# Kernel tuning notes

Hardware: AMD Instinct MI355X
Metric: run time of the kernel (lower is better)

## Reference

```python
import jax, jax.numpy as jnp
import numpy as np

N = 100000       # num nodes
E = 1600000      # num edges
D_IN = 32
D_HID = 32
D_OUT = 32
K = 3            # Chebyshev order (number of terms)


def setup_inputs() -> dict:
    key = jax.random.key(0)
    k1, k2, k3, k4, k5, k6 = jax.random.split(key, 6)
    x = jax.random.normal(k1, (N, D_IN), dtype=jnp.float32)
    edge_index = jax.random.randint(k2, (2, E), 0, N, dtype=jnp.int64)
    s1 = 1.0 / np.sqrt(D_IN)
    s2 = 1.0 / np.sqrt(D_HID)
    W1 = jax.random.uniform(k3, (K, D_IN, D_HID), jnp.float32, -s1, s1)
    b1 = jax.random.uniform(k4, (D_HID,), jnp.float32, -s1, s1)
    W2 = jax.random.uniform(k5, (K, D_HID, D_OUT), jnp.float32, -s2, s2)
    b2 = jax.random.uniform(k6, (D_OUT,), jnp.float32, -s2, s2)
    return {"x": x, "edge_index": edge_index, "W1": W1, "b1": b1, "W2": W2, "b2": b2}


def _prop(x, row, col, w):
    # L_hat @ x : gather along col, scale by edge weight, scatter-add to row.
    # (diagonal of the rescaled Laplacian cancels to 0 in PyG ChebConv with
    #  sym normalization and lambda_max=2, so only off-diagonal edges remain)
    return jax.ops.segment_sum(w[:, None] * x[col], row, num_segments=N)


def _cheb_conv(x, row, col, w, W, b):
    # Chebyshev recurrence: Tx0 = x, Tx1 = L_hat x, Tx_k = 2 L_hat Tx_{k-1} - Tx_{k-2}
    k_terms = W.shape[0]
    Tx0 = x
    out = Tx0 @ W[0]
    if k_terms > 1:
        Tx1 = _prop(Tx0, row, col, w)
        out = out + Tx1 @ W[1]
        for k in range(2, k_terms):
            Tx2 = 2.0 * _prop(Tx1, row, col, w) - Tx0
            out = out + Tx2 @ W[k]
            Tx0, Tx1 = Tx1, Tx2
    return out + b


def reference(x, edge_index, W1, b1, W2, b2):
    row, col = edge_index[0], edge_index[1]
    mask = (row != col).astype(x.dtype)            # remove_self_loops
    deg = jax.ops.segment_sum(mask, row, num_segments=N)
    dinv = jnp.where(deg > 0, 1.0 / jnp.sqrt(jnp.maximum(deg, 1.0)), 0.0)
    w = -mask * dinv[row] * dinv[col]              # scaled Laplacian off-diagonal weights
    x0 = x
    h = jax.nn.relu(_cheb_conv(x, row, col, w, W1, b1))
    h = _cheb_conv(h, row, col, w, W2, b2)
    return h + x0
```

## Files before the change

kernel.cpp:

```cpp
#include <hip/hip_runtime.h>

#define NN 100000
#define EE 1600000
#define DD 32
#define NBUK 391
#define BROWS 256
#define TILE 4096
#define NT 391
#define BCAP2 4864

#define TOTP   106176
#define ENT2SZ 2084352
#define ZTOT   ((TOTP * 16 + ENT2SZ * 4) / 16)
#define ZPB    ((ZTOT + NT - 1) / NT)

__constant__ int c_cap[9]   = {0, 2944, 56320, 43520, 2944, 256, 64, 64, 64};
__constant__ int c_pbase[9] = {0, 0, 2944, 59264, 102784, 105728, 105984, 106048, 106112};
__constant__ int c_ebase[9] = {0, 0, 23552, 924672, 1969152, 2063360, 2073600, 2076672, 2080256};

typedef unsigned int uint;
typedef unsigned short ushort;
typedef unsigned char uchar;
typedef __attribute__((ext_vector_type(8))) short bf16x8;
typedef __attribute__((ext_vector_type(4))) float f32x4;
typedef __attribute__((ext_vector_type(2))) float f32x2;

typedef __attribute__((ext_vector_type(4))) uint u32x4v;
typedef __attribute__((ext_vector_type(2))) uint u32x2v;
typedef __attribute__((ext_vector_type(4))) int i32x4v;
typedef __attribute__((ext_vector_type(4))) float f32x4v;

__device__ __forceinline__ uint4 ntld(const uint4* p) {
    u32x4v v = __builtin_nontemporal_load((const u32x4v*)p);
    uint4 r; r.x = v.x; r.y = v.y; r.z = v.z; r.w = v.w; return r;
}
__device__ __forceinline__ uint2 ntld(const uint2* p) {
    u32x2v v = __builtin_nontemporal_load((const u32x2v*)p);
    uint2 r; r.x = v.x; r.y = v.y; return r;
}
__device__ __forceinline__ int4 ntld(const int4* p) {
    i32x4v v = __builtin_nontemporal_load((const i32x4v*)p);
    int4 r; r.x = v.x; r.y = v.y; r.z = v.z; r.w = v.w; return r;
}
__device__ __forceinline__ float4 ntld(const float4* p) {
    f32x4v v = __builtin_nontemporal_load((const f32x4v*)p);
    float4 r; r.x = v.x; r.y = v.y; r.z = v.z; r.w = v.w; return r;
}
__device__ __forceinline__ int   ntld(const int* p)   { return __builtin_nontemporal_load(p); }
__device__ __forceinline__ float ntld(const float* p) { return __builtin_nontemporal_load(p); }
__device__ __forceinline__ void ntst(uint4* p, uint4 v) {
    u32x4v w; w.x = v.x; w.y = v.y; w.z = v.z; w.w = v.w;
    __builtin_nontemporal_store(w, (u32x4v*)p);
}
__device__ __forceinline__ void ntst(int4* p, int4 v) {
    uint4 u; u.x = (uint)v.x; u.y = (uint)v.y; u.z = (uint)v.z; u.w = (uint)v.w;
    ntst((uint4*)p, u);
}
__device__ __forceinline__ void ntst(uint2* p, uint2 v) {
    u32x2v w; w.x = v.x; w.y = v.y;
    __builtin_nontemporal_store(w, (u32x2v*)p);
}
__device__ __forceinline__ void ntst(int* p, int v)     { __builtin_nontemporal_store(v, p); }
__device__ __forceinline__ void ntst(float* p, float v) { __builtin_nontemporal_store(v, p); }

__device__ __forceinline__ ushort f2b(float f) {
    uint u = __float_as_uint(f);
    u += 0x7fffu + ((u >> 16) & 1u);
    return (ushort)(u >> 16);
}
__device__ __forceinline__ uint f2e4(float f) {
    uint u = __float_as_uint(f);
    uint s = (u >> 24) & 0x80u;
    float a = fabsf(f) * 0x1p-120f;
    uint g = __float_as_uint(a);
    g += 0x7FFFFu + ((g >> 20) & 1u);
    uint m = g >> 20;
    if (m > 0x7Eu) m = 0x7Eu;
    return s | m;
}
__device__ __forceinline__ bf16x8 as_bf16x8(uint4 v) {
    union { uint4 u; bf16x8 b; } cv; cv.u = v; return cv.b;
}
__device__ __forceinline__ void acc8(float* acc, uint2 v) {
#pragma unroll
    for (int wi = 0; wi < 2; ++wi) {
        uint w = (&v.x)[wi];
        f32x2 lo = __builtin_amdgcn_cvt_pk_f32_fp8((int)w, false);
        f32x2 hi = __builtin_amdgcn_cvt_pk_f32_fp8((int)w, true);
        acc[wi * 4 + 0] += lo.x;
        acc[wi * 4 + 1] += lo.y;
        acc[wi * 4 + 2] += hi.x;
        acc[wi * 4 + 3] += hi.y;
    }
}


__global__ void k_part(const int* __restrict__ ei, int* __restrict__ gtail,
                       int* __restrict__ pairs, uint4* __restrict__ zbase) {
    {
        int z0 = blockIdx.x * ZPB;
        int ze = z0 + ZPB; if (ze > ZTOT) ze = ZTOT;
        uint4 zz; zz.x = 0; zz.y = 0; zz.z = 0; zz.w = 0;
        for (int i = z0 + threadIdx.x; i < ze; i += 256) ntst(zbase + i, zz);
    }
    __shared__ int hist[512];
    __shared__ int gbase[512];
    int t = threadIdx.x;
    hist[t] = 0; hist[t + 256] = 0;
    __syncthreads();
    int e0 = blockIdx.x * TILE;
    int pk[16], rk[16], bb[16];
#pragma unroll
    for (int k = 0; k < 16; ++k) {
        int e = e0 + t + k * 256;
        bb[k] = -1;
        if (e < EE) {
            int r = ntld(ei + e), c = ntld(ei + EE + e);
            if (r != c) {
                bb[k] = r >> 8;
                pk[k] = (r & (BROWS - 1)) | (c << 8);
                rk[k] = atomicAdd(&hist[bb[k]], 1);
            }
        }
    }
    __syncthreads();
    for (int q = t; q < NBUK; q += 256) {
        int cnt = hist[q];
        gbase[q] = cnt ? atomicAdd(&gtail[q * 16], cnt) : 0;
    }
    __syncthreads();
#pragma unroll
    for (int k = 0; k < 16; ++k) {
        if (bb[k] >= 0) {
            int pos = gbase[bb[k]] + rk[k];
            if (pos < BCAP2) pairs[bb[k] * BCAP2 + pos] = pk[k];
        }
    }
}


__global__ void k_build2(const int* __restrict__ gtail, const int* __restrict__ pairs,
                         float* __restrict__ dinv, int* __restrict__ ctail,
                         int* __restrict__ ent2, int4* __restrict__ pdesc,
                         const float* __restrict__ x, uint2* __restrict__ xb,
                         uint* __restrict__ xb8,
                         const float* __restrict__ W1, const float* __restrict__ W2,
                         ushort* __restrict__ wb1, ushort* __restrict__ wb2,
                         uint* __restrict__ t1b8, uint* __restrict__ hb8) {
    if (blockIdx.x == NBUK) {
        for (int i = threadIdx.x; i < 6144; i += 256) {
            const float* W = W1; ushort* wb = wb1;
            int ii = i;
            if (ii >= 3072) { ii -= 3072; W = W2; wb = wb2; }
            int term = ii >> 10, rem = ii & 1023;
            int h = rem >> 9, lane = (rem >> 3) & 63, j = rem & 7;
            int k = ((lane >> 4) << 3) + j;
            int col = (h << 4) | (lane & 15);
            float val = W[term * 1024 + k * 32 + col];
            if (term == 0) val -= W[2 * 1024 + k * 32 + col];
            wb[ii] = f2b(val);
        }
        if (threadIdx.x >= 64 && threadIdx.x < 72) xb8[NN * 8 + threadIdx.x - 64] = 0;
        if (threadIdx.x >= 72 && threadIdx.x < 80) t1b8[NN * 8 + threadIdx.x - 72] = 0;
        if (threadIdx.x >= 80 && threadIdx.x < 88) hb8[NN * 8 + threadIdx.x - 80] = 0;
        return;
    }
    __shared__ int lcnt[BROWS];
    __shared__ int lh[16];
    __shared__ int gb[16];
    __shared__ int sofs[BROWS];
    __shared__ float sdinv[BROWS];
    __shared__ uchar scls[BROWS];
    __shared__ int slab[BROWS * 64];
    int b = blockIdx.x, t = threadIdx.x;
    lcnt[t] = 0;
    if (t < 16) lh[t] = 0;
    for (int i = t; i < BROWS * 64; i += 256) slab[i] = NN;
    __syncthreads();
    int cnt = gtail[b * 16]; if (cnt > BCAP2) cnt = BCAP2;
    const int* pp = pairs + b * BCAP2;
    for (int i = t; i < cnt; i += 256) {
        int v = ntld(pp + i);
        int lr = v & (BROWS - 1);
        int pos = atomicAdd(&lcnt[lr], 1);
        if (pos < 64) slab[(lr << 6) + pos] = (int)((uint)v >> 8);
    }
    __syncthreads();
    int n = b * BROWS + t;
    int cpl = 0, lrank = 0;
    float dv = 0.0f;
    if (n < NN) {
        int d = lcnt[t];
        int ms = d > 64 ? 64 : d;
        int cls = (ms + 7) >> 3;
        cpl = cls ? cls : 1;
        dv = d > 0 ? rsqrtf((float)d) : 0.0f;
        dinv[n] = dv;
        lrank = atomicAdd(&lh[cpl], 1);
    }
    sdinv[t] = dv;
    __syncthreads();
    if (t < 16) gb[t] = lh[t] ? atomicAdd(&ctail[t], lh[t]) : 0;
    __syncthreads();
    int myofs = -1;
    if (n < NN) {
        int rank = gb[cpl] + lrank;
        if (rank < c_cap[cpl]) {
            myofs = c_ebase[cpl] + rank * (cpl << 3);
            int4 pv; pv.x = n; pv.y = cpl; pv.z = (int)__float_as_uint(dv); pv.w = 0;
            pdesc[c_pbase[cpl] + rank] = pv;
        }
    }
    sofs[t] = myofs;
    scls[t] = (uchar)cpl;
    __syncthreads();
    for (int i = t; i < BROWS * 16; i += 256) {
        int row = i >> 4, piece = i & 15;
        int ofs = sofs[row];
        if (ofs >= 0 && piece < (scls[row] << 1)) {
            int4 v = *(const int4*)&slab[(row << 6) + (piece << 2)];
            ntst((int4*)&ent2[ofs + (piece << 2)], v);
        }
    }
    int base4 = b * 2048;
    for (int i = t; i < 2048; i += 256) {
        int row = i >> 3;
        if (b * BROWS + row < NN) {
            float4 v = ntld((const float4*)x + base4 + i);
            uint2 b2;
            b2.x = (uint)f2b(v.x) | ((uint)f2b(v.y) << 16);
            b2.y = (uint)f2b(v.z) | ((uint)f2b(v.w) << 16);
            ntst(xb + base4 + i, b2);
            float dvr = sdinv[row];
            xb8[base4 + i] = f2e4(dvr * v.x) | (f2e4(dvr * v.y) << 8)
                           | (f2e4(dvr * v.z) << 16) | (f2e4(dvr * v.w) << 24);
        }
    }
}


__global__ void k_prop(const int4* __restrict__ pdesc, const int* __restrict__ ent2,
                       const uint2* __restrict__ src8d,
                       uint2* __restrict__ dst8d,
                       uint4* __restrict__ dstbq) {
    int tid = blockIdx.x * blockDim.x + threadIdx.x;
    int g = tid >> 3;
    int sub = tid & 3, h = (tid >> 2) & 1;
    int4 pd = ntld(pdesc + g);
    constexpr int kPB[9] = {0, 0, 2944, 59264, 102784, 105728, 105984, 106048, 106112};
    constexpr int kEB[9] = {0, 0, 23552, 924672, 1969152, 2063360, 2073600, 2076672, 2080256};
    int cls = 1, pb = 0, eb = 0;
#pragma unroll
    for (int c = 2; c <= 8; ++c)
        if (g >= kPB[c]) { cls = c; pb = kPB[c]; eb = kEB[c]; }
    const int* ep = ent2 + eb + (g - pb) * (cls << 3);
    int mr = cls << 3;
    float acc[8] = {0, 0, 0, 0, 0, 0, 0, 0};
    for (int i = h * 8; i < mr; i += 16) {
        uint4 C0 = ntld((const uint4*)(ep + i));
        uint4 C1 = ntld((const uint4*)(ep + i + 4));
        uint2 v0 = src8d[(C0.x << 2) + sub];
        uint2 v1 = src8d[(C0.y << 2) + sub];
        uint2 v2 = src8d[(C0.z << 2) + sub];
        uint2 v3 = src8d[(C0.w << 2) + sub];
        uint2 v4 = src8d[(C1.x << 2) + sub];
        uint2 v5 = src8d[(C1.y << 2) + sub];
        uint2 v6 = src8d[(C1.z << 2) + sub];
        uint2 v7 = src8d[(C1.w << 2) + sub];
        acc8(acc, v0); acc8(acc, v1); acc8(acc, v2); acc8(acc, v3);
        acc8(acc, v4); acc8(acc, v5); acc8(acc, v6); acc8(acc, v7);
    }
    if (pd.y == 0) return;
    int n = pd.x;
    float dn = __uint_as_float((uint)pd.z);
    float s = -dn;
#pragma unroll
    for (int k = 0; k < 8; ++k)
        acc[k] = s * (acc[k] + __shfl_xor(acc[k], 4, 64));
    if (h == 0) {
        uint4 ob;
#pragma unroll
        for (int wi = 0; wi < 4; ++wi)
            (&ob.x)[wi] = (uint)f2b(acc[wi * 2]) | ((uint)f2b(acc[wi * 2 + 1]) << 16);
        ntst(dstbq + (n << 2) + sub, ob);
    } else {
        uint2 o8;
        o8.x = f2e4(dn * acc[0]) | (f2e4(dn * acc[1]) << 8)
             | (f2e4(dn * acc[2]) << 16) | (f2e4(dn * acc[3]) << 24);
        o8.y = f2e4(dn * acc[4]) | (f2e4(dn * acc[5]) << 8)
             | (f2e4(dn * acc[6]) << 16) | (f2e4(dn * acc[7]) << 24);
        ntst(dst8d + (n << 2) + sub, o8);
    }
}


__global__ void __launch_bounds__(256) k_prop2c(
        const int4* __restrict__ pdesc, const int* __restrict__ ent2,
        const uint2* __restrict__ src8d,
        const uint4* __restrict__ t0g,
        const uint4* __restrict__ t1g,
        const ushort* __restrict__ wb, const float* __restrict__ bias,
        const float* __restrict__ residf, float* __restrict__ outf,
        ushort* __restrict__ outb, uchar* __restrict__ outb8, int do_relu) {
    __shared__ ushort sT[32 * 40];
    __shared__ int   sn[32];
    __shared__ float sdv[32];
    int tid = blockIdx.x * 256 + threadIdx.x;
    int g = tid >> 3, sub = tid & 3, h = (tid >> 2) & 1;
    int slot = threadIdx.x >> 3;
    int4 pd = ntld(pdesc + g);
    constexpr int kPB[9] = {0, 0, 2944, 59264, 102784, 105728, 105984, 106048, 106112};
    constexpr int kEB[9] = {0, 0, 23552, 924672, 1969152, 2063360, 2073600, 2076672, 2080256};
    int cls = 1, pb = 0, eb = 0;
#pragma unroll
    for (int c = 2; c <= 8; ++c)
        if (g >= kPB[c]) { cls = c; pb = kPB[c]; eb = kEB[c]; }
    const int* ep = ent2 + eb + (g - pb) * (cls << 3);
    int mr = cls << 3;
    float acc[8] = {0, 0, 0, 0, 0, 0, 0, 0};
    for (int i = h * 8; i < mr; i += 16) {
        uint4 C0 = ntld((const uint4*)(ep + i));
        uint4 C1 = ntld((const uint4*)(ep + i + 4));
        uint2 v0 = src8d[(C0.x << 2) + sub];
        uint2 v1 = src8d[(C0.y << 2) + sub];
        uint2 v2 = src8d[(C0.z << 2) + sub];
        uint2 v3 = src8d[(C0.w << 2) + sub];
        uint2 v4 = src8d[(C1.x << 2) + sub];
        uint2 v5 = src8d[(C1.y << 2) + sub];
        uint2 v6 = src8d[(C1.z << 2) + sub];
        uint2 v7 = src8d[(C1.w << 2) + sub];
        acc8(acc, v0); acc8(acc, v1); acc8(acc, v2); acc8(acc, v3);
        acc8(acc, v4); acc8(acc, v5); acc8(acc, v6); acc8(acc, v7);
    }
    if (pd.y != 0) {
        float dn = __uint_as_float((uint)pd.z);
        float s = -2.0f * dn;
#pragma unroll
        for (int k = 0; k < 8; ++k)
            acc[k] = s * (acc[k] + __shfl_xor(acc[k], 4, 64));
        if (h == 0) {
            uint4 ow;
#pragma unroll
            for (int wi = 0; wi < 4; ++wi)
                (&ow.x)[wi] = (uint)f2b(acc[wi * 2]) | ((uint)f2b(acc[wi * 2 + 1]) << 16);
            *(uint4*)&sT[slot * 40 + sub * 8] = ow;
            if (sub == 0) { sn[slot] = pd.x; sdv[slot] = dn; }
        }
    } else if ((threadIdx.x & 7) == 0) {
        sn[slot] = -1;
    }
    __syncthreads();
    if (threadIdx.x >= 128) return;
    int wv = threadIdx.x >> 6, lane = threadIdx.x & 63;
    int q = lane >> 4, lr = lane & 15;
    const uint4* wq = (const uint4*)wb;
    bf16x8 bf[3][2];
#pragma unroll
    for (int t = 0; t < 3; ++t)
#pragma unroll
        for (int hh = 0; hh < 2; ++hh)
            bf[t][hh] = as_bf16x8(wq[((t * 2 + hh) << 6) + lane]);
    float bias0 = bias[lr], bias1 = bias[16 + lr];
    uint4 z; z.x = 0; z.y = 0; z.z = 0; z.w = 0;
    int lrow = wv * 16 + lr;
    int an = sn[lrow];
    bool ok = an >= 0;
    int ai = (an << 2) + q;
    bf16x8 a0 = as_bf16x8(ok ? ntld(t0g + ai) : z);
    bf16x8 a1 = as_bf16x8(ok ? ntld(t1g + ai) : z);
    bf16x8 a2 = *(const bf16x8*)&sT[lrow * 40 + q * 8];
    f32x4 c0 = {0.f, 0.f, 0.f, 0.f};
    f32x4 c1 = {0.f, 0.f, 0.f, 0.f};
    c0 = __builtin_amdgcn_mfma_f32_16x16x32_bf16(a0, bf[0][0], c0, 0, 0, 0);
    c0 = __builtin_amdgcn_mfma_f32_16x16x32_bf16(a1, bf[1][0], c0, 0, 0, 0);
    c0 = __builtin_amdgcn_mfma_f32_16x16x32_bf16(a2, bf[2][0], c0, 0, 0, 0);
    c1 = __builtin_amdgcn_mfma_f32_16x16x32_bf16(a0, bf[0][1], c1, 0, 0, 0);
    c1 = __builtin_amdgcn_mfma_f32_16x16x32_bf16(a1, bf[1][1], c1, 0, 0, 0);
    c1 = __builtin_amdgcn_mfma_f32_16x16x32_bf16(a2, bf[2][1], c1, 0, 0, 0);
#pragma unroll
    for (int r = 0; r < 4; ++r) {
        int ls = wv * 16 + (q << 2) + r;
        int nd = sn[ls];
        if (nd < 0) continue;
        float v0 = c0[r] + bias0;
        float v1 = c1[r] + bias1;
        if (do_relu) { v0 = fmaxf(v0, 0.0f); v1 = fmaxf(v1, 0.0f); }
        if (outb) {
            float dvv = sdv[ls];
            outb[nd * DD + lr] = f2b(v0);
            outb[nd * DD + 16 + lr] = f2b(v1);
            outb8[nd * DD + lr] = (uchar)f2e4(dvv * v0);
            outb8[nd * DD + 16 + lr] = (uchar)f2e4(dvv * v1);
        } else {
            ntst(outf + nd * DD + lr, v0 + ntld(residf + nd * DD + lr));
            ntst(outf + nd * DD + 16 + lr, v1 + ntld(residf + nd * DD + 16 + lr));
        }
    }
}


extern "C" void kernel_launch(void* const* d_in, const int* in_sizes, int n_in,
                              void* d_out, int out_size, void* d_ws, size_t ws_size,
                              hipStream_t stream) {
    const float* x  = (const float*)d_in[0];
    const int*   ei = (const int*)d_in[1];
    const float* W1 = (const float*)d_in[2];
    const float* b1 = (const float*)d_in[3];
    const float* W2 = (const float*)d_in[4];
    const float* b2 = (const float*)d_in[5];
    float* out = (float*)d_out;

    char* wsp = (char*)d_ws;
    size_t off = 0;
    auto take = [&](size_t bytes) {
        char* p = wsp + off;
        off = (off + bytes + 255) & ~(size_t)255;
        return p;
    };
    int*    ctrl  = (int*)take((size_t)(NBUK * 16 + 16) * 4);
    int*    gtail = ctrl;
    int*    ctail = ctrl + NBUK * 16;
    int4*   pdesc = (int4*)take((size_t)TOTP * 16);
    int*    ent2  = (int*)take((size_t)ENT2SZ * 4);
    float*  dinv  = (float*)take((size_t)NN * 4);
    ushort* wb1   = (ushort*)take((size_t)3072 * 2);
    ushort* wb2   = (ushort*)take((size_t)3072 * 2);
    int*    pairs = (int*)take((size_t)NBUK * BCAP2 * 4);
    ushort* xb    = (ushort*)take((size_t)NN * DD * 2);
    ushort* t1b   = (ushort*)take((size_t)NN * DD * 2);
    ushort* hb    = (ushort*)take((size_t)NN * DD * 2);
    uchar*  xb8   = (uchar*)take((size_t)(NN + 1) * DD);
    uchar*  t1b8  = (uchar*)take((size_t)(NN + 1) * DD);
    uchar*  hb8   = (uchar*)take((size_t)(NN + 1) * DD);

    hipMemsetAsync(ctrl, 0, (size_t)(NBUK * 16 + 16) * 4, stream);

    k_part  <<<NT, 256, 0, stream>>>(ei, gtail, pairs, (uint4*)pdesc);
    k_build2<<<NBUK + 1, 256, 0, stream>>>(gtail, pairs, dinv, ctail, ent2, pdesc,
                                           x, (uint2*)xb, (uint*)xb8,
                                           W1, W2, wb1, wb2,
                                           (uint*)t1b8, (uint*)hb8);

    const int pgrid = TOTP * 8 / 256;
    k_prop  <<<pgrid, 256, 0, stream>>>(pdesc, ent2, (const uint2*)xb8,
                                        (uint2*)t1b8, (uint4*)t1b);
    k_prop2c<<<pgrid, 256, 0, stream>>>(pdesc, ent2, (const uint2*)t1b8,
                                        (const uint4*)xb, (const uint4*)t1b,
                                        wb1, b1, nullptr, nullptr,
                                        hb, hb8, 1);
    k_prop  <<<pgrid, 256, 0, stream>>>(pdesc, ent2, (const uint2*)hb8,
                                        (uint2*)t1b8, (uint4*)t1b);
    k_prop2c<<<pgrid, 256, 0, stream>>>(pdesc, ent2, (const uint2*)t1b8,
                                        (const uint4*)hb, (const uint4*)t1b,
                                        wb2, b2, x, out,
                                        nullptr, nullptr, 0);
}
```

Measured before the change: 218.8 us.

## Replace global atomic bucket partition with per-tile local sort and offset table

The edge partition kernel now sorts each tile's edges by destination bucket in shared memory, using a block-wide prefix scan. It writes them contiguously per tile together with a per-bucket offset table, replacing global atomicAdd tails into fixed-capacity bucket arrays. The build kernel then gathers each bucket's slice from every tile, which removes the memset launch, the global atomics and the BCAP2 overflow cap. It also drops the unused dinv global write and zeroes ctail inside k_part. The cost is that build now issues 391 small, serial, per-thread strided segment reads, which may load poorly compared to the old contiguous reads.

```diff
diff --git a/kernel.cpp b/kernel.cpp
--- a/kernel.cpp
+++ b/kernel.cpp
@@ -7,7 +7,6 @@
 #define BROWS 256
 #define TILE 4096
 #define NT 391
-#define BCAP2 4864
 
 #define TOTP   106176
 #define ENT2SZ 2084352
@@ -95,16 +94,20 @@
 }
 
 
-__global__ void k_part(const int* __restrict__ ei, int* __restrict__ gtail,
-                       int* __restrict__ pairs, uint4* __restrict__ zbase) {
+__global__ void k_part(const int* __restrict__ ei, int* __restrict__ pairs2,
+                       ushort* __restrict__ ofs, uint4* __restrict__ zbase,
+                       int* __restrict__ ctail) {
     {
         int z0 = blockIdx.x * ZPB;
         int ze = z0 + ZPB; if (ze > ZTOT) ze = ZTOT;
         uint4 zz; zz.x = 0; zz.y = 0; zz.z = 0; zz.w = 0;
         for (int i = z0 + threadIdx.x; i < ze; i += 256) ntst(zbase + i, zz);
     }
+    if (blockIdx.x == 0 && threadIdx.x < 16) ctail[threadIdx.x] = 0;
     __shared__ int hist[512];
-    __shared__ int gbase[512];
+    __shared__ int h2[256];
+    __shared__ int pref[512];
+    __shared__ int spk[TILE];
     int t = threadIdx.x;
     hist[t] = 0; hist[t + 256] = 0;
     __syncthreads();
@@ -124,23 +127,34 @@
         }
     }
     __syncthreads();
-    for (int q = t; q < NBUK; q += 256) {
-        int cnt = hist[q];
-        gbase[q] = cnt ? atomicAdd(&gtail[q * 16], cnt) : 0;
-    }
-    __syncthreads();
-#pragma unroll
-    for (int k = 0; k < 16; ++k) {
-        if (bb[k] >= 0) {
-            int pos = gbase[bb[k]] + rk[k];
-            if (pos < BCAP2) pairs[bb[k] * BCAP2 + pos] = pk[k];
-        }
-    }
-}
-
-
-__global__ void k_build2(const int* __restrict__ gtail, const int* __restrict__ pairs,
-                         float* __restrict__ dinv, int* __restrict__ ctail,
+    int a = hist[2 * t], b = hist[2 * t + 1];
+    h2[t] = a + b;
+    __syncthreads();
+    for (int d = 1; d < 256; d <<= 1) {
+        int v = h2[t];
+        int u = (t >= d) ? h2[t - d] : 0;
+        __syncthreads();
+        h2[t] = v + u;
+        __syncthreads();
+    }
+    int base = t ? h2[t - 1] : 0;
+    pref[2 * t] = base;
+    pref[2 * t + 1] = base + a;
+    __syncthreads();
+#pragma unroll
+    for (int k = 0; k < 16; ++k)
+        if (bb[k] >= 0) spk[pref[bb[k]] + rk[k]] = pk[k];
+    for (int q = t; q <= NBUK; q += 256)
+        ofs[q * NT + blockIdx.x] = (ushort)pref[q];
+    __syncthreads();
+    int tot = pref[NBUK];
+    int* dst = pairs2 + blockIdx.x * TILE;
+    for (int i = t; i < tot; i += 256) ntst(dst + i, spk[i]);
+}
+
+
+__global__ void k_build2(const int* __restrict__ pairs2, const ushort* __restrict__ ofs,
+                         int* __restrict__ ctail,
                          int* __restrict__ ent2, int4* __restrict__ pdesc,
                          const float* __restrict__ x, uint2* __restrict__ xb,
                          uint* __restrict__ xb8,
@@ -171,19 +185,26 @@
     __shared__ int sofs[BROWS];
     __shared__ float sdinv[BROWS];
     __shared__ uchar scls[BROWS];
+    __shared__ ushort so0[NT], so1[NT];
     __shared__ int slab[BROWS * 64];
     int b = blockIdx.x, t = threadIdx.x;
     lcnt[t] = 0;
     if (t < 16) lh[t] = 0;
+    for (int i = t; i < NT; i += 256) {
+        so0[i] = ofs[b * NT + i];
+        so1[i] = ofs[(b + 1) * NT + i];
+    }
     for (int i = t; i < BROWS * 64; i += 256) slab[i] = NN;
     __syncthreads();
-    int cnt = gtail[b * 16]; if (cnt > BCAP2) cnt = BCAP2;
-    const int* pp = pairs + b * BCAP2;
-    for (int i = t; i < cnt; i += 256) {
-        int v = ntld(pp + i);
-        int lr = v & (BROWS - 1);
-        int pos = atomicAdd(&lcnt[lr], 1);
-        if (pos < 64) slab[(lr << 6) + pos] = (int)((uint)v >> 8);
+    for (int tt = t; tt < NT; tt += 256) {
+        int s = so0[tt], e = so1[tt];
+        const int* pp = pairs2 + tt * TILE;
+        for (int i = s; i < e; ++i) {
+            int v = ntld(pp + i);
+            int lr = v & (BROWS - 1);
+            int pos = atomicAdd(&lcnt[lr], 1);
+            if (pos < 64) slab[(lr << 6) + pos] = (int)((uint)v >> 8);
+        }
     }
     __syncthreads();
     int n = b * BROWS + t;
@@ -195,7 +216,6 @@
         int cls = (ms + 7) >> 3;
         cpl = cls ? cls : 1;
         dv = d > 0 ? rsqrtf((float)d) : 0.0f;
-        dinv[n] = dv;
         lrank = atomicAdd(&lh[cpl], 1);
     }
     sdinv[t] = dv;
@@ -216,10 +236,10 @@
     __syncthreads();
     for (int i = t; i < BROWS * 16; i += 256) {
         int row = i >> 4, piece = i & 15;
-        int ofs = sofs[row];
-        if (ofs >= 0 && piece < (scls[row] << 1)) {
+        int ofs2 = sofs[row];
+        if (ofs2 >= 0 && piece < (scls[row] << 1)) {
             int4 v = *(const int4*)&slab[(row << 6) + (piece << 2)];
-            ntst((int4*)&ent2[ofs + (piece << 2)], v);
+            ntst((int4*)&ent2[ofs2 + (piece << 2)], v);
         }
     }
     int base4 = b * 2048;
@@ -417,26 +437,23 @@
         off = (off + bytes + 255) & ~(size_t)255;
         return p;
     };
-    int*    ctrl  = (int*)take((size_t)(NBUK * 16 + 16) * 4);
-    int*    gtail = ctrl;
-    int*    ctail = ctrl + NBUK * 16;
-    int4*   pdesc = (int4*)take((size_t)TOTP * 16);
-    int*    ent2  = (int*)take((size_t)ENT2SZ * 4);
-    float*  dinv  = (float*)take((size_t)NN * 4);
-    ushort* wb1   = (ushort*)take((size_t)3072 * 2);
-    ushort* wb2   = (ushort*)take((size_t)3072 * 2);
-    int*    pairs = (int*)take((size_t)NBUK * BCAP2 * 4);
-    ushort* xb    = (ushort*)take((size_t)NN * DD * 2);
-    ushort* t1b   = (ushort*)take((size_t)NN * DD * 2);
-    ushort* hb    = (ushort*)take((size_t)NN * DD * 2);
-    uchar*  xb8   = (uchar*)take((size_t)(NN + 1) * DD);
-    uchar*  t1b8  = (uchar*)take((size_t)(NN + 1) * DD);
-    uchar*  hb8   = (uchar*)take((size_t)(NN + 1) * DD);
-
-    hipMemsetAsync(ctrl, 0, (size_t)(NBUK * 16 + 16) * 4, stream);
-
-    k_part  <<<NT, 256, 0, stream>>>(ei, gtail, pairs, (uint4*)pdesc);
-    k_build2<<<NBUK + 1, 256, 0, stream>>>(gtail, pairs, dinv, ctail, ent2, pdesc,
+    int*    ctail  = (int*)take((size_t)16 * 4);
+    int4*   pdesc  = (int4*)take((size_t)TOTP * 16);
+    int*    ent2   = (int*)take((size_t)ENT2SZ * 4);
+    ushort* ofs    = (ushort*)take((size_t)(NBUK + 1) * NT * 2);
+    int*    pairs2 = (int*)take((size_t)NT * TILE * 4);
+    ushort* wb1    = (ushort*)take((size_t)3072 * 2);
+    ushort* wb2    = (ushort*)take((size_t)3072 * 2);
+    ushort* xb     = (ushort*)take((size_t)NN * DD * 2);
+    ushort* t1b    = (ushort*)take((size_t)NN * DD * 2);
+    ushort* hb     = (ushort*)take((size_t)NN * DD * 2);
+    uchar*  xb8    = (uchar*)take((size_t)(NN + 1) * DD);
+    uchar*  t1b8   = (uchar*)take((size_t)(NN + 1) * DD);
+    uchar*  hb8    = (uchar*)take((size_t)(NN + 1) * DD);
+
+
+    k_part  <<<NT, 256, 0, stream>>>(ei, pairs2, ofs, (uint4*)pdesc, ctail);
+    k_build2<<<NBUK + 1, 256, 0, stream>>>(pairs2, ofs, ctail, ent2, pdesc,
                                            x, (uint2*)xb, (uint*)xb8,
                                            W1, W2, wb1, wb2,
                                            (uint*)t1b8, (uint*)hb8);
```

Measured after the change: 221.4 us. No clear change (+1.2%).
